# Optimization experiments

Measured on AMD Instinct MI355X. Metric: run time of the kernel, lower is better.

Reference implementation:

```python
import jax, jax.numpy as jnp
import numpy as np

B, T, H, IN, D = 256, 64, 256, 2, 8

def _gru_cell(x, h, Wih, Whh, bih, bhh):
    gi = x @ Wih.T + bih          # [B,3H]
    gh = h @ Whh.T + bhh
    ir, iz, inn = jnp.split(gi, 3, axis=-1)
    hr, hz, hn = jnp.split(gh, 3, axis=-1)
    r = jax.nn.sigmoid(ir + hr)
    z = jax.nn.sigmoid(iz + hz)
    n = jnp.tanh(inn + r * hn)
    return (1.0 - z) * n + z * h

def _gru2(x, h, p):
    # h: [2,B,H]; p: 8-tuple of layer-0 then layer-1 GRU params
    h0 = _gru_cell(x, h[0], p[0], p[1], p[2], p[3])
    h1 = _gru_cell(h0, h[1], p[4], p[5], p[6], p[7])
    return jnp.stack([h0, h1], axis=0)

def _attend(h_new, buf, i, attn_W, v_W, fc_W, fc_b):
    # h_new: [2,B,H] fresh RNN hidden; buf: [B,T,2,H] history of hiddens
    s = h_new.transpose(1, 0, 2)                            # [B,2,H]
    es = jnp.einsum('blh,gh->blg', s, attn_W[:, :H])        # s half of cat(s,hiddens)
    eh = jnp.einsum('bjlh,gh->bjlg', buf, attn_W[:, H:])    # hiddens half
    energy = jnp.tanh(es[:, None] + eh)                     # [B,T,2,H]
    logits = jnp.einsum('bjlg,og->bjlo', energy, v_W)       # [B,T,2,2]
    mask = (jnp.arange(buf.shape[1]) <= i)[None, :, None, None]
    logits = jnp.where(mask, logits, jnp.float32(-1e30))
    m = logits.max(axis=(1, 2), keepdims=True)              # softmax over all 2*(i+1) history slots
    e = jnp.exp(logits - m)
    a = e / e.sum(axis=(1, 2), keepdims=True)
    c = jnp.einsum('bjlo,bjlh->obh', a, buf)                # [2,B,H] == bmm(a,hiddens).transpose(0,1)
    h_cat = jnp.concatenate([c, h_new], axis=-1)            # [2,B,2H]
    return h_cat @ fc_W.T + fc_b                            # [2,B,H]

def setup_inputs():
    key = jax.random.key(0)
    ks = jax.random.split(key, 32)
    def u(k, shape, fan):
        b = 1.0 / np.sqrt(fan)
        return jax.random.uniform(k, shape, jnp.float32, -b, b)
    inp = {'received': jax.random.normal(ks[0], (B, T, IN), jnp.float32)}
    i = 1
    for g in ('g1', 'g2'):
        inp[g + '_Wih0'] = u(ks[i], (3 * H, IN), H); i += 1
        inp[g + '_Whh0'] = u(ks[i], (3 * H, H), H); i += 1
        inp[g + '_bih0'] = u(ks[i], (3 * H,), H); i += 1
        inp[g + '_bhh0'] = u(ks[i], (3 * H,), H); i += 1
        inp[g + '_Wih1'] = u(ks[i], (3 * H, H), H); i += 1
        inp[g + '_Whh1'] = u(ks[i], (3 * H, H), H); i += 1
        inp[g + '_bih1'] = u(ks[i], (3 * H,), H); i += 1
        inp[g + '_bhh1'] = u(ks[i], (3 * H,), H); i += 1
    inp['fc_W'] = u(ks[i], (H, 2 * H), 2 * H); i += 1
    inp['fc_b'] = u(ks[i], (H,), 2 * H); i += 1
    inp['attn_W'] = u(ks[i], (H, 2 * H), 2 * H); i += 1
    inp['v_W'] = u(ks[i], (2, H), H); i += 1
    inp['out_W'] = u(ks[i], (1, 2 * H), 2 * H); i += 1
    inp['out_b'] = u(ks[i], (1,), 2 * H); i += 1
    return inp

def reference(received, g1_Wih0, g1_Whh0, g1_bih0, g1_bhh0, g1_Wih1, g1_Whh1, g1_bih1, g1_bhh1,
              g2_Wih0, g2_Whh0, g2_bih0, g2_bhh0, g2_Wih1, g2_Whh1, g2_bih1, g2_bhh1,
              fc_W, fc_b, attn_W, v_W, out_W, out_b):
    p1 = (g1_Wih0, g1_Whh0, g1_bih0, g1_bhh0, g1_Wih1, g1_Whh1, g1_bih1, g1_bhh1)
    p2 = (g2_Wih0, g2_Whh0, g2_bih0, g2_bhh0, g2_Wih1, g2_Whh1, g2_bih1, g2_bhh1)
    b, t = received.shape[0], received.shape[1]
    h_init = jnp.zeros((2, b, H), received.dtype)
    buf_init = jnp.zeros((b, t, 2, H), received.dtype)

    def step(carry, inp):
        h1, h2, b1, b2 = carry
        x, i = inp
        h1n = _gru2(x, h1, p1)
        h2n = _gru2(x, h2, p2)
        b1 = b1.at[:, i].set(h1n.transpose(1, 0, 2))
        b2 = b2.at[:, i].set(h2n.transpose(1, 0, 2))
        h1a = _attend(h1n, b1, i, attn_W, v_W, fc_W, fc_b)
        h2a = _attend(h2n, b2, i, attn_W, v_W, fc_W, fc_b)
        return (h1a, h2a, b1, b2), (h1n[1], h2n[1])

    xs = (received.transpose(1, 0, 2), jnp.arange(t))
    _, (o1, o2) = jax.lax.scan(step, (h_init, h_init, buf_init, buf_init), xs)
    out1 = o1.transpose(1, 0, 2)   # [B,T,H] = concat of per-step top-layer GRU outputs
    out2 = o2.transpose(1, 0, 2)
    ar = jnp.arange(t)
    idx = jnp.where(ar >= t - D - 1, t - 1, ar + D)   # delayed stream-2 features
    rnn_out = jnp.concatenate([out1, out2[:, idx]], axis=-1)  # [B,T,2H]
    return jax.nn.sigmoid(rnn_out @ out_W.T + out_b)          # [B,T,1]
```

## Files before the change

### kernel.cpp

```cpp
#include <hip/hip_runtime.h>

#define BATCH 256
#define TT    64
#define HH    256
#define DD    8

#define BW    4
#define NTHR  1024
#define NBLK  (2 * (BATCH / BW))

#define CH48  24576
#define CH32  16384

typedef __attribute__((ext_vector_type(8))) short bfrag;
typedef __attribute__((ext_vector_type(4))) float f4;
typedef __attribute__((ext_vector_type(4))) unsigned int uv4;

#define SWZ(g) ((((g) & 31) << 3) | ((g) >> 5))

__device__ __forceinline__ float rcpf(float x) { return __builtin_amdgcn_rcpf(x); }
__device__ __forceinline__ float sigf(float x) { return rcpf(1.0f + __expf(-x)); }
__device__ __forceinline__ float tanh_fast(float x) {
  const float e = __expf(-2.0f * x);
  return __builtin_fmaf(2.0f, rcpf(1.0f + e), -1.0f);
}
__device__ __forceinline__ unsigned short f2bf(float f) {
  union { float f; unsigned int u; } v; v.f = f;
  return (unsigned short)((v.u + 0x7fffu + ((v.u >> 16) & 1u)) >> 16);
}
__device__ __forceinline__ float bf_lo(unsigned int u) {
  union { unsigned int u; float f; } v; v.u = u << 16; return v.f;
}
__device__ __forceinline__ float bf_hi(unsigned int u) {
  union { unsigned int u; float f; } v; v.u = u & 0xffff0000u; return v.f;
}
__device__ __forceinline__ bfrag zero_frag() {
  bfrag r;
#pragma unroll
  for (int x = 0; x < 8; x++) r[x] = 0;
  return r;
}
__device__ __forceinline__ f4 mfma16(bfrag a, bfrag b, f4 c) {
  return __builtin_amdgcn_mfma_f32_16x16x32_bf16(a, b, c, 0, 0, 0);
}

__device__ __forceinline__ void wait_vm(int n) {
  if (n == 0)      asm volatile("s_waitcnt vmcnt(0)" ::: "memory");
  else if (n == 2) asm volatile("s_waitcnt vmcnt(2)" ::: "memory");
  else if (n == 3) asm volatile("s_waitcnt vmcnt(3)" ::: "memory");
  else if (n == 6) asm volatile("s_waitcnt vmcnt(6)" ::: "memory");
  else             asm volatile("s_waitcnt vmcnt(7)" ::: "memory");
  __builtin_amdgcn_sched_barrier(0);
}
__device__ __forceinline__ void lds_release_bar() {
  asm volatile("s_waitcnt lgkmcnt(0)" ::: "memory");
  __builtin_amdgcn_sched_barrier(0);
  __builtin_amdgcn_s_barrier();
  __builtin_amdgcn_sched_barrier(0);
}

__device__ __forceinline__ void gl_lds16(const unsigned short* g, unsigned short* l) {
  __builtin_amdgcn_global_load_lds(
      (const __attribute__((address_space(1))) unsigned int*)g,
      (__attribute__((address_space(3))) unsigned int*)l, 16, 0, 0);
}
__device__ __forceinline__ void stage48(const unsigned short* g, unsigned short* l,
                                        int wave, int lane) {
#pragma unroll
  for (int r = 0; r < 3; ++r)
    gl_lds16(g + wave * 1536 + r * 512 + lane * 8, l + wave * 1536 + r * 512);
}
__device__ __forceinline__ void stage32(const unsigned short* g, unsigned short* l,
                                        int wave, int lane) {
#pragma unroll
  for (int r = 0; r < 2; ++r)
    gl_lds16(g + wave * 1024 + r * 512 + lane * 8, l + wave * 1024 + r * 512);
}

#define W1_ELEMS  196608
#define STACK_W   (3 * W1_ELEMS)
#define B3_OFF    (2 * STACK_W)
#define B4_OFF    (B3_OFF + 131072)
#define WF_TOTAL  (B4_OFF + 131072)

__global__ __launch_bounds__(256) void prep_weights(
    const float* __restrict__ g1_Whh0, const float* __restrict__ g1_Wih1, const float* __restrict__ g1_Whh1,
    const float* __restrict__ g2_Whh0, const float* __restrict__ g2_Wih1, const float* __restrict__ g2_Whh1,
    const float* __restrict__ attn_W, const float* __restrict__ fc_W,
    unsigned short* __restrict__ wf) {
  const int id = blockIdx.x * 256 + threadIdx.x;
  if (id >= WF_TOTAL) return;
  float src;
  if (id < 2 * STACK_W) {
    const int s = id / STACK_W, r = id % STACK_W;
    const int mm = r / W1_ELEMS, e = r % W1_ELEMS;
    const int c = e / CH48, e2 = e % CH48;
    const int wg = e2 >> 9, l8 = e2 & 511;
    const int w = wg / 3, g = wg % 3;
    const int lane = l8 >> 3, j = l8 & 7;
    const int n = w * 16 + (lane & 15);
    const int k = c * 32 + ((lane >> 4) << 3) + j;
    const float* W = (mm == 0) ? (s ? g2_Whh0 : g1_Whh0)
                   : (mm == 1) ? (s ? g2_Wih1 : g1_Wih1)
                               : (s ? g2_Whh1 : g1_Whh1);
    src = W[(g * 256 + n) * 256 + k];
  } else if (id < B4_OFF) {
    const int e = id - B3_OFF;
    const int c = e / CH32, e2 = e % CH32;
    const int t = e2 >> 9, l8 = e2 & 511;
    const int lane = l8 >> 3, j = l8 & 7;
    const int n = t * 16 + (lane & 15);
    const int k = c * 32 + ((lane >> 4) << 3) + j;
    src = (n < 256) ? attn_W[n * 512 + k] : attn_W[(n - 256) * 512 + 256 + k];
  } else {
    const int e = id - B4_OFF;
    const int cc = e / CH32, e2 = e % CH32;
    const int w = e2 >> 10, c2 = (e2 >> 9) & 1, l8 = e2 & 511;
    const int lane = l8 >> 3, j = l8 & 7;
    const int c = cc * 2 + c2;
    const int n = w * 16 + (lane & 15);
    const int k = c * 32 + ((lane >> 4) << 3) + j;
    src = fc_W[n * 512 + k];
  }
  wf[id] = f2bf(src);
}

__global__ __launch_bounds__(NTHR) void gru_attn(
    const float* __restrict__ received,
    const float* __restrict__ g1_Wih0, const float* __restrict__ g1_bih0, const float* __restrict__ g1_bhh0,
    const float* __restrict__ g1_bih1, const float* __restrict__ g1_bhh1,
    const float* __restrict__ g2_Wih0, const float* __restrict__ g2_bih0, const float* __restrict__ g2_bhh0,
    const float* __restrict__ g2_bih1, const float* __restrict__ g2_bhh1,
    const float* __restrict__ fc_b, const float* __restrict__ v_W, const float* __restrict__ out_W,
    const unsigned short* __restrict__ wf,
    unsigned short* __restrict__ buf_g, unsigned short* __restrict__ ehb_g,
    float* __restrict__ ws_p) {
  const int tid  = threadIdx.x;
  const int lane = tid & 63, wave = tid >> 6;
  const int col  = lane & 15, q = lane >> 4;
  const int s    = blockIdx.x & 1;
  const int b0   = (blockIdx.x >> 1) * BW;

  const float* Wih0 = s ? g2_Wih0 : g1_Wih0;
  const float* bih0 = s ? g2_bih0 : g1_bih0;
  const float* bhh0 = s ? g2_bhh0 : g1_bhh0;
  const float* bih1 = s ? g2_bih1 : g1_bih1;
  const float* bhh1 = s ? g2_bhh1 : g1_bhh1;

  const unsigned short* SR = wf + (size_t)s * STACK_W;
  const unsigned short* B3 = wf + B3_OFF;
  const unsigned short* B4 = wf + B4_OFF;

  unsigned short* buf = buf_g + (size_t)s * BATCH * TT * 2 * HH;
  unsigned short* ehb = ehb_g + (size_t)s * BATCH * TT * 2 * HH;
  float* pp = ws_p + (size_t)s * BATCH * TT;

  const int nm0 = wave * 16 + col;
  const float wxr0 = Wih0[nm0 * 2],         wxr1 = Wih0[nm0 * 2 + 1];
  const float wxz0 = Wih0[(256 + nm0) * 2], wxz1 = Wih0[(256 + nm0) * 2 + 1];
  const float wxn0 = Wih0[(512 + nm0) * 2], wxn1 = Wih0[(512 + nm0) * 2 + 1];
  const float br0  = bih0[nm0] + bhh0[nm0];
  const float bz0  = bih0[256 + nm0] + bhh0[256 + nm0];
  const float bni0 = bih0[512 + nm0], bnh0 = bhh0[512 + nm0];
  const float br1  = bih1[nm0] + bhh1[nm0];
  const float bz1  = bih1[256 + nm0] + bhh1[256 + nm0];
  const float bni1 = bih1[512 + nm0], bnh1 = bhh1[512 + nm0];
  const float fcb  = fc_b[nm0];
  const float owv  = out_W[s * HH + nm0];

  __shared__ float          hf[8 * 260] __attribute__((aligned(16)));
  __shared__ unsigned short hb[8 * 264] __attribute__((aligned(16)));
  __shared__ unsigned short hnb[8 * 264] __attribute__((aligned(16)));
  __shared__ float          es_s[8 * 264] __attribute__((aligned(16)));
  __shared__ unsigned short cacb[8 * 264] __attribute__((aligned(16)));
  __shared__ float          lp[TT * 4 * 2 * 2];
  __shared__ float          vw_s[512];
  __shared__ float          cpart[2 * 2 * 4 * 256] __attribute__((aligned(16)));
  __shared__ float          pw_s[64];
  __shared__ float          sinv_s[8];
  __shared__ float          xv_s[BW * TT * 2];
  __shared__ unsigned short wbuf[2][CH48] __attribute__((aligned(16)));

  for (int x = tid; x < 8 * 260; x += NTHR) hf[x] = 0.0f;
  for (int x = tid; x < 8 * 264; x += NTHR) hb[x] = 0;
  if (tid < 512) { const int o = tid >> 8, g = tid & 255; vw_s[o * 256 + SWZ(g)] = v_W[tid]; }
  if (tid < BW * TT * 2) {
    const int b = tid >> 7, r = tid & 127;
    xv_s[tid] = received[(size_t)(b0 + b) * TT * 2 + r];
  }
  __syncthreads();

  stage48(SR + 0 * CH48, wbuf[0], wave, lane);
  stage48(SR + 1 * CH48, wbuf[1], wave, lane);

#pragma unroll 1
  for (int i = 0; i < TT; ++i) {
    f4 aR = {0,0,0,0}, aZ = {0,0,0,0}, aN = {0,0,0,0};
#pragma unroll
    for (int c = 0; c < 8; ++c) {
      wait_vm(3);
      __builtin_amdgcn_s_barrier();
      __builtin_amdgcn_sched_barrier(0);
      const unsigned short* wb = wbuf[c & 1];
      const bfrag av = (col < BW) ? *(const bfrag*)&hb[col * 264 + c * 32 + q * 8] : zero_frag();
      const bfrag f0 = *(const bfrag*)&wb[(wave * 3 + 0) * 512 + lane * 8];
      const bfrag f1 = *(const bfrag*)&wb[(wave * 3 + 1) * 512 + lane * 8];
      const bfrag f2 = *(const bfrag*)&wb[(wave * 3 + 2) * 512 + lane * 8];
      aR = mfma16(av, f0, aR); aZ = mfma16(av, f1, aZ); aN = mfma16(av, f2, aN);
      lds_release_bar();
      stage48(SR + (c + 2) * CH48, wbuf[c & 1], wave, lane);
    }
    if (lane < 16) {
#pragma unroll
      for (int reg = 0; reg < 4; reg++) {
        const int b = reg;
        const float xr = xv_s[(b * TT + i) * 2 + 0];
        const float xi = xv_s[(b * TT + i) * 2 + 1];
        const float rr = sigf(xr * wxr0 + xi * wxr1 + br0 + aR[reg]);
        const float zz = sigf(xr * wxz0 + xi * wxz1 + bz0 + aZ[reg]);
        const float nn = tanh_fast(xr * wxn0 + xi * wxn1 + bni0 + rr * (aN[reg] + bnh0));
        const float hn0 = (1.0f - zz) * nn + zz * hf[b * 260 + nm0];
        const unsigned short hv = f2bf(hn0);
        hnb[b * 264 + nm0] = hv;
        buf[((size_t)(b0 + b) * (TT * 2) + i * 2 + 0) * HH + nm0] = hv;
      }
    }
    lds_release_bar();

    f4 iR = {0,0,0,0}, iZ = {0,0,0,0}, iN = {0,0,0,0};
#pragma unroll
    for (int c = 8; c < 16; ++c) {
      wait_vm(c < 10 ? 7 : 3);
      __builtin_amdgcn_s_barrier();
      __builtin_amdgcn_sched_barrier(0);
      const unsigned short* wb = wbuf[c & 1];
      const bfrag av = (col < BW) ? *(const bfrag*)&hnb[col * 264 + (c - 8) * 32 + q * 8] : zero_frag();
      const bfrag f0 = *(const bfrag*)&wb[(wave * 3 + 0) * 512 + lane * 8];
      const bfrag f1 = *(const bfrag*)&wb[(wave * 3 + 1) * 512 + lane * 8];
      const bfrag f2 = *(const bfrag*)&wb[(wave * 3 + 2) * 512 + lane * 8];
      iR = mfma16(av, f0, iR); iZ = mfma16(av, f1, iZ); iN = mfma16(av, f2, iN);
      lds_release_bar();
      stage48(SR + (c + 2) * CH48, wbuf[c & 1], wave, lane);
    }

    f4 hR = {0,0,0,0}, hZ = {0,0,0,0}, hN = {0,0,0,0};
#pragma unroll
    for (int c = 16; c < 24; ++c) {
      wait_vm(c < 23 ? 3 : 0);
      __builtin_amdgcn_s_barrier();
      __builtin_amdgcn_sched_barrier(0);
      const unsigned short* wb = wbuf[c & 1];
      const bfrag av = (col < BW) ? *(const bfrag*)&hb[(4 + col) * 264 + (c - 16) * 32 + q * 8] : zero_frag();
      const bfrag f0 = *(const bfrag*)&wb[(wave * 3 + 0) * 512 + lane * 8];
      const bfrag f1 = *(const bfrag*)&wb[(wave * 3 + 1) * 512 + lane * 8];
      const bfrag f2 = *(const bfrag*)&wb[(wave * 3 + 2) * 512 + lane * 8];
      hR = mfma16(av, f0, hR); hZ = mfma16(av, f1, hZ); hN = mfma16(av, f2, hN);
      lds_release_bar();
      if (c + 2 < 24) stage48(SR + (c + 2) * CH48, wbuf[c & 1], wave, lane);
    }
    stage32(B3 + 0 * CH32, wbuf[0], wave, lane);
    stage32(B3 + 1 * CH32, wbuf[1], wave, lane);
    {
      float pv[4] = {0.f, 0.f, 0.f, 0.f};
      if (lane < 16) {
#pragma unroll
        for (int reg = 0; reg < 4; reg++) {
          const int b = reg;
          const float rr = sigf(iR[reg] + hR[reg] + br1);
          const float zz = sigf(iZ[reg] + hZ[reg] + bz1);
          const float nn = tanh_fast(iN[reg] + bni1 + rr * (hN[reg] + bnh1));
          const float hn1 = (1.0f - zz) * nn + zz * hf[(4 + b) * 260 + nm0];
          const unsigned short hv = f2bf(hn1);
          hnb[(4 + b) * 264 + nm0] = hv;
          buf[((size_t)(b0 + b) * (TT * 2) + i * 2 + 1) * HH + nm0] = hv;
          pv[reg] += hn1 * owv;
        }
      }
#pragma unroll
      for (int reg = 0; reg < 4; reg++) {
#pragma unroll
        for (int d = 1; d < 16; d <<= 1) pv[reg] += __shfl_xor(pv[reg], d, 64);
      }
      if (lane == 0) {
#pragma unroll
        for (int reg = 0; reg < 4; reg++) pw_s[wave * 4 + reg] = pv[reg];
      }
    }
    lds_release_bar();

    {
      f4 ac0 = {0,0,0,0}, ac1 = {0,0,0,0};
#pragma unroll
      for (int c = 0; c < 8; ++c) {
        wait_vm(c < 2 ? 6 : (c < 7 ? 2 : 0));
        __builtin_amdgcn_s_barrier();
        __builtin_amdgcn_sched_barrier(0);
        const unsigned short* wb = wbuf[c & 1];
        const bfrag av = (col < 8) ? *(const bfrag*)&hnb[col * 264 + c * 32 + q * 8] : zero_frag();
        const bfrag f0 = *(const bfrag*)&wb[(2 * wave + 0) * 512 + lane * 8];
        const bfrag f1 = *(const bfrag*)&wb[(2 * wave + 1) * 512 + lane * 8];
        ac0 = mfma16(av, f0, ac0);
        ac1 = mfma16(av, f1, ac1);
        lds_release_bar();
        if (c + 2 < 8) stage32(B3 + (c + 2) * CH32, wbuf[c & 1], wave, lane);
      }
#pragma unroll
      for (int tt = 0; tt < 2; tt++) {
        const f4 acc = tt ? ac1 : ac0;
        const int t = wave * 2 + tt;
        if (lane < 32) {
          const int n = t * 16 + col;
#pragma unroll
          for (int reg = 0; reg < 4; reg++) {
            const int m = q * 4 + reg;
            const int l = m >> 2, b = m & 3;
            if (t < 16) es_s[(b * 2 + l) * 264 + SWZ(n)] = acc[reg];
            else ehb[((size_t)(b0 + b) * (TT * 2) + i * 2 + l) * HH + (n - 256)] = f2bf(acc[reg]);
          }
        }
      }
      if (tid < 4) {
        float ss = 0.0f;
#pragma unroll
        for (int w = 0; w < 16; w++) ss += pw_s[w * 4 + tid];
        pp[(size_t)(b0 + tid) * TT + i] = ss;
      }
    }
    __syncthreads();

    {
      const int nslot = 64 * (i + 1);
      int slot = tid;
      uv4 cur[4];
      if (slot < nslot) {
        const uv4* ep = (const uv4*)(ehb + ((size_t)(b0 + ((slot >> 3) & 3)) * (TT * 2) +
                                            (slot >> 6) * 2 + ((slot >> 5) & 1)) * HH + (slot & 7) * 32);
#pragma unroll
        for (int u = 0; u < 4; u++) cur[u] = __builtin_nontemporal_load(ep + u);
      }
      for (; slot < nslot; slot += NTHR) {
        const int snext = slot + NTHR;
        uv4 nxt[4];
        if (snext < nslot) {
          const uv4* ep2 = (const uv4*)(ehb + ((size_t)(b0 + ((snext >> 3) & 3)) * (TT * 2) +
                                               (snext >> 6) * 2 + ((snext >> 5) & 1)) * HH + (snext & 7) * 32);
#pragma unroll
          for (int u = 0; u < 4; u++) nxt[u] = __builtin_nontemporal_load(ep2 + u);
        } else {
#pragma unroll
          for (int u = 0; u < 4; u++) nxt[u] = cur[u];
        }
        const int g8 = slot & 7;
        const int b  = (slot >> 3) & 3;
        const int l  = (slot >> 5) & 1;
        const int j  = slot >> 6;
        const int eb = (b * 2 + l) * 264;
        float l0 = 0.0f, l1 = 0.0f;
#pragma unroll
        for (int u = 0; u < 4; u++) {
#pragma unroll
          for (int k = 0; k < 4; k++) {
            const int m = u * 8 + k * 2;
            const float e0 = tanh_fast(es_s[eb + (m * 8 + g8)] + bf_lo(cur[u][k]));
            const float e1 = tanh_fast(es_s[eb + ((m + 1) * 8 + g8)] + bf_hi(cur[u][k]));
            l0 = fmaf(e0, vw_s[m * 8 + g8], fmaf(e1, vw_s[(m + 1) * 8 + g8], l0));
            l1 = fmaf(e0, vw_s[256 + m * 8 + g8], fmaf(e1, vw_s[256 + (m + 1) * 8 + g8], l1));
          }
        }
#pragma unroll
        for (int d = 1; d < 8; d <<= 1) { l0 += __shfl_xor(l0, d, 64); l1 += __shfl_xor(l1, d, 64); }
        if (g8 == 0) {
          lp[((j * 4 + b) * 2 + l) * 2 + 0] = __expf(l0);
          lp[((j * 4 + b) * 2 + l) * 2 + 1] = __expf(l1);
        }
#pragma unroll
        for (int u = 0; u < 4; u++) cur[u] = nxt[u];
      }
    }
    __syncthreads();

    {
      if (wave < 8) {
        const int b = wave >> 1, o = wave & 1;
        const int jl2 = 2 * (i + 1);
        const int jl0 = lane, jl1 = lane + 64;
        float sa = 0.0f;
        if (jl0 < jl2) sa += lp[((jl0 >> 1) * 4 + b) * 4 + (jl0 & 1) * 2 + o];
        if (jl1 < jl2) sa += lp[((jl1 >> 1) * 4 + b) * 4 + (jl1 & 1) * 2 + o];
#pragma unroll
        for (int d = 1; d < 64; d <<= 1) sa += __shfl_xor(sa, d, 64);
        if (lane == 0) sinv_s[b * 2 + o] = rcpf(sa);
      }
      const int h2   = tid & 127;
      const int jpar = (tid >> 7) & 1;
      const int cb   = tid >> 8;
      const unsigned int* bp = (const unsigned int*)(buf + ((size_t)(b0 + cb) * (TT * 2)) * HH);
      float c00 = 0.f, c01 = 0.f, c10 = 0.f, c11 = 0.f;
      unsigned int aj0 = 0, aj1 = 0, bj0 = 0, bj1 = 0;
      int j = jpar;
      if (j <= i) {
        aj0 = __builtin_nontemporal_load(bp + (j * 2 + 0) * 128 + h2);
        aj1 = __builtin_nontemporal_load(bp + (j * 2 + 1) * 128 + h2);
        bj0 = __builtin_nontemporal_load(bp + ((j + 2) * 2 + 0) * 128 + h2);
        bj1 = __builtin_nontemporal_load(bp + ((j + 2) * 2 + 1) * 128 + h2);
      }
      for (; j <= i; j += 2) {
        unsigned int cj0 = 0, cj1 = 0;
        if (j + 4 <= i) {
          cj0 = __builtin_nontemporal_load(bp + ((j + 4) * 2 + 0) * 128 + h2);
          cj1 = __builtin_nontemporal_load(bp + ((j + 4) * 2 + 1) * 128 + h2);
        }
#pragma unroll
        for (int l = 0; l < 2; l++) {
          const unsigned int u = l ? aj1 : aj0;
          const float e0 = lp[((j * 4 + cb) * 2 + l) * 2 + 0];
          const float e1 = lp[((j * 4 + cb) * 2 + l) * 2 + 1];
          const float v0 = bf_lo(u), v1 = bf_hi(u);
          c00 = fmaf(e0, v0, c00); c01 = fmaf(e0, v1, c01);
          c10 = fmaf(e1, v0, c10); c11 = fmaf(e1, v1, c11);
        }
        aj0 = bj0; aj1 = bj1; bj0 = cj0; bj1 = cj1;
      }
      ((float2*)&cpart[((jpar * 2 + 0) * 4 + cb) * 256])[h2] = make_float2(c00, c01);
      ((float2*)&cpart[((jpar * 2 + 1) * 4 + cb) * 256])[h2] = make_float2(c10, c11);
    }
    __syncthreads();

    stage32(B4 + 0 * CH32, wbuf[0], wave, lane);
    stage32(B4 + 1 * CH32, wbuf[1], wave, lane);
    for (int x = tid; x < 2 * BW * HH; x += NTHR) {
      const int g = x & 255, b = (x >> 8) & 3, o = x >> 10;
      const float v = (cpart[((0 * 2 + o) * 4 + b) * 256 + g] +
                       cpart[((1 * 2 + o) * 4 + b) * 256 + g]) *
                      sinv_s[b * 2 + o];
      cacb[(o * 4 + b) * 264 + g] = f2bf(v);
    }
    __syncthreads();

    {
      f4 acc = {0, 0, 0, 0};
#pragma unroll
      for (int cc = 0; cc < 8; ++cc) {
        wait_vm(cc < 7 ? 2 : 0);
        __builtin_amdgcn_s_barrier();
        __builtin_amdgcn_sched_barrier(0);
        const unsigned short* wb = wbuf[cc & 1];
        bfrag a0v, a1v;
        if (col < 8) {
          a0v = (cc < 4) ? *(const bfrag*)&cacb[col * 264 + cc * 64 + q * 8]
                         : *(const bfrag*)&hnb[col * 264 + (cc - 4) * 64 + q * 8];
          a1v = (cc < 4) ? *(const bfrag*)&cacb[col * 264 + cc * 64 + 32 + q * 8]
                         : *(const bfrag*)&hnb[col * 264 + (cc - 4) * 64 + 32 + q * 8];
        } else { a0v = zero_frag(); a1v = zero_frag(); }
        const bfrag g0 = *(const bfrag*)&wb[(wave * 2 + 0) * 512 + lane * 8];
        const bfrag g1 = *(const bfrag*)&wb[(wave * 2 + 1) * 512 + lane * 8];
        acc = mfma16(a0v, g0, acc);
        acc = mfma16(a1v, g1, acc);
        lds_release_bar();
        if (cc + 2 < 8) stage32(B4 + (cc + 2) * CH32, wbuf[cc & 1], wave, lane);
      }
      if (i + 1 < TT) {
        stage48(SR + 0 * CH48, wbuf[0], wave, lane);
        stage48(SR + 1 * CH48, wbuf[1], wave, lane);
      }
      if (lane < 32) {
#pragma unroll
        for (int reg = 0; reg < 4; reg++) {
          const int m = q * 4 + reg;
          const float v = acc[reg] + fcb;
          hf[m * 260 + nm0] = v;
          hb[m * 264 + nm0] = f2bf(v);
        }
      }
    }
    lds_release_bar();
  }
}

__global__ __launch_bounds__(256) void final_combine(const float* __restrict__ ws_p,
                                                     const float* __restrict__ out_b,
                                                     float* __restrict__ out) {
  const int gidx = blockIdx.x * blockDim.x + threadIdx.x;
  if (gidx >= BATCH * TT) return;
  const int b = gidx >> 6;
  const int t = gidx & 63;
  const int idx = (t >= TT - DD - 1) ? (TT - 1) : (t + DD);
  const float* p1 = ws_p;
  const float* p2 = ws_p + (size_t)BATCH * TT;
  const float v = p1[(size_t)b * TT + t] + p2[(size_t)b * TT + idx] + out_b[0];
  out[gidx] = 1.0f / (1.0f + __expf(-v));
}

extern "C" void kernel_launch(void* const* d_in, const int* in_sizes, int n_in,
                              void* d_out, int out_size, void* d_ws, size_t ws_size,
                              hipStream_t stream) {
  const float* received = (const float*)d_in[0];
  const float* g1_Wih0 = (const float*)d_in[1];
  const float* g1_Whh0 = (const float*)d_in[2];
  const float* g1_bih0 = (const float*)d_in[3];
  const float* g1_bhh0 = (const float*)d_in[4];
  const float* g1_Wih1 = (const float*)d_in[5];
  const float* g1_Whh1 = (const float*)d_in[6];
  const float* g1_bih1 = (const float*)d_in[7];
  const float* g1_bhh1 = (const float*)d_in[8];
  const float* g2_Wih0 = (const float*)d_in[9];
  const float* g2_Whh0 = (const float*)d_in[10];
  const float* g2_bih0 = (const float*)d_in[11];
  const float* g2_bhh0 = (const float*)d_in[12];
  const float* g2_Wih1 = (const float*)d_in[13];
  const float* g2_Whh1 = (const float*)d_in[14];
  const float* g2_bih1 = (const float*)d_in[15];
  const float* g2_bhh1 = (const float*)d_in[16];
  const float* fc_W   = (const float*)d_in[17];
  const float* fc_b   = (const float*)d_in[18];
  const float* attn_W = (const float*)d_in[19];
  const float* v_W    = (const float*)d_in[20];
  const float* out_W  = (const float*)d_in[21];
  const float* out_b  = (const float*)d_in[22];

  float* ws_p = (float*)d_ws;
  unsigned short* buf = (unsigned short*)(ws_p + 2 * BATCH * TT);
  unsigned short* ehb = buf + (size_t)2 * BATCH * TT * 2 * HH;
  unsigned short* wf  = ehb + (size_t)2 * BATCH * TT * 2 * HH;

  hipLaunchKernelGGL(prep_weights, dim3((WF_TOTAL + 255) / 256), dim3(256), 0, stream,
                     g1_Whh0, g1_Wih1, g1_Whh1, g2_Whh0, g2_Wih1, g2_Whh1,
                     attn_W, fc_W, wf);

  hipLaunchKernelGGL(gru_attn, dim3(NBLK), dim3(NTHR), 0, stream,
                     received,
                     g1_Wih0, g1_bih0, g1_bhh0, g1_bih1, g1_bhh1,
                     g2_Wih0, g2_bih0, g2_bhh0, g2_bih1, g2_bhh1,
                     fc_b, v_W, out_W, wf, buf, ehb, ws_p);

  hipLaunchKernelGGL(final_combine, dim3((BATCH * TT + 255) / 256), dim3(256), 0, stream,
                     ws_p, out_b, (float*)d_out);
}
```

Baseline: 6.193 ms.

## Drop per-chunk workgroup barriers in weight streaming and deepen history prefetch

Removes the s_barrier and LDS-release barrier around every weight chunk in the GRU and FC MFMA loops. This relies on each wave staging and consuming only its own slice of the double-buffered LDS weights, so only per-wave vmcnt waits remain. The next-stage weight prefetches now start after the block-wide barriers instead of before them, which keeps them from overwriting buffers other waves may still be reading. Separately, the attention-context loop now keeps four history rows of nontemporal loads in flight instead of two, and several __syncthreads become lighter LDS release barriers. The risk is a cross-wave race if any wave reads LDS data that another wave staged.

```diff
diff --git a/kernel.cpp b/kernel.cpp
--- a/kernel.cpp
+++ b/kernel.cpp
@@ -48,7 +48,6 @@
   if (n == 0)      asm volatile("s_waitcnt vmcnt(0)" ::: "memory");
   else if (n == 2) asm volatile("s_waitcnt vmcnt(2)" ::: "memory");
   else if (n == 3) asm volatile("s_waitcnt vmcnt(3)" ::: "memory");
-  else if (n == 6) asm volatile("s_waitcnt vmcnt(6)" ::: "memory");
   else             asm volatile("s_waitcnt vmcnt(7)" ::: "memory");
   __builtin_amdgcn_sched_barrier(0);
 }
@@ -199,15 +198,13 @@
 #pragma unroll
     for (int c = 0; c < 8; ++c) {
       wait_vm(3);
-      __builtin_amdgcn_s_barrier();
-      __builtin_amdgcn_sched_barrier(0);
       const unsigned short* wb = wbuf[c & 1];
       const bfrag av = (col < BW) ? *(const bfrag*)&hb[col * 264 + c * 32 + q * 8] : zero_frag();
       const bfrag f0 = *(const bfrag*)&wb[(wave * 3 + 0) * 512 + lane * 8];
       const bfrag f1 = *(const bfrag*)&wb[(wave * 3 + 1) * 512 + lane * 8];
       const bfrag f2 = *(const bfrag*)&wb[(wave * 3 + 2) * 512 + lane * 8];
       aR = mfma16(av, f0, aR); aZ = mfma16(av, f1, aZ); aN = mfma16(av, f2, aN);
-      lds_release_bar();
+      __builtin_amdgcn_sched_barrier(0);
       stage48(SR + (c + 2) * CH48, wbuf[c & 1], wave, lane);
     }
     if (lane < 16) {
@@ -231,15 +228,13 @@
 #pragma unroll
     for (int c = 8; c < 16; ++c) {
       wait_vm(c < 10 ? 7 : 3);
-      __builtin_amdgcn_s_barrier();
-      __builtin_amdgcn_sched_barrier(0);
       const unsigned short* wb = wbuf[c & 1];
       const bfrag av = (col < BW) ? *(const bfrag*)&hnb[col * 264 + (c - 8) * 32 + q * 8] : zero_frag();
       const bfrag f0 = *(const bfrag*)&wb[(wave * 3 + 0) * 512 + lane * 8];
       const bfrag f1 = *(const bfrag*)&wb[(wave * 3 + 1) * 512 + lane * 8];
       const bfrag f2 = *(const bfrag*)&wb[(wave * 3 + 2) * 512 + lane * 8];
       iR = mfma16(av, f0, iR); iZ = mfma16(av, f1, iZ); iN = mfma16(av, f2, iN);
-      lds_release_bar();
+      __builtin_amdgcn_sched_barrier(0);
       stage48(SR + (c + 2) * CH48, wbuf[c & 1], wave, lane);
     }
 
@@ -247,19 +242,15 @@
 #pragma unroll
     for (int c = 16; c < 24; ++c) {
       wait_vm(c < 23 ? 3 : 0);
-      __builtin_amdgcn_s_barrier();
-      __builtin_amdgcn_sched_barrier(0);
       const unsigned short* wb = wbuf[c & 1];
       const bfrag av = (col < BW) ? *(const bfrag*)&hb[(4 + col) * 264 + (c - 16) * 32 + q * 8] : zero_frag();
       const bfrag f0 = *(const bfrag*)&wb[(wave * 3 + 0) * 512 + lane * 8];
       const bfrag f1 = *(const bfrag*)&wb[(wave * 3 + 1) * 512 + lane * 8];
       const bfrag f2 = *(const bfrag*)&wb[(wave * 3 + 2) * 512 + lane * 8];
       hR = mfma16(av, f0, hR); hZ = mfma16(av, f1, hZ); hN = mfma16(av, f2, hN);
-      lds_release_bar();
+      __builtin_amdgcn_sched_barrier(0);
       if (c + 2 < 24) stage48(SR + (c + 2) * CH48, wbuf[c & 1], wave, lane);
     }
-    stage32(B3 + 0 * CH32, wbuf[0], wave, lane);
-    stage32(B3 + 1 * CH32, wbuf[1], wave, lane);
     {
       float pv[4] = {0.f, 0.f, 0.f, 0.f};
       if (lane < 16) {
@@ -287,21 +278,21 @@
       }
     }
     lds_release_bar();
+    stage32(B3 + 0 * CH32, wbuf[0], wave, lane);
+    stage32(B3 + 1 * CH32, wbuf[1], wave, lane);
 
     {
       f4 ac0 = {0,0,0,0}, ac1 = {0,0,0,0};
 #pragma unroll
       for (int c = 0; c < 8; ++c) {
-        wait_vm(c < 2 ? 6 : (c < 7 ? 2 : 0));
-        __builtin_amdgcn_s_barrier();
-        __builtin_amdgcn_sched_barrier(0);
+        wait_vm(c < 7 ? 2 : 0);
         const unsigned short* wb = wbuf[c & 1];
         const bfrag av = (col < 8) ? *(const bfrag*)&hnb[col * 264 + c * 32 + q * 8] : zero_frag();
         const bfrag f0 = *(const bfrag*)&wb[(2 * wave + 0) * 512 + lane * 8];
         const bfrag f1 = *(const bfrag*)&wb[(2 * wave + 1) * 512 + lane * 8];
         ac0 = mfma16(av, f0, ac0);
         ac1 = mfma16(av, f1, ac1);
-        lds_release_bar();
+        __builtin_amdgcn_sched_barrier(0);
         if (c + 2 < 8) stage32(B3 + (c + 2) * CH32, wbuf[c & 1], wave, lane);
       }
 #pragma unroll
@@ -377,7 +368,7 @@
         for (int u = 0; u < 4; u++) cur[u] = nxt[u];
       }
     }
-    __syncthreads();
+    lds_release_bar();
 
     {
       if (wave < 8) {
@@ -396,35 +387,41 @@
       const int cb   = tid >> 8;
       const unsigned int* bp = (const unsigned int*)(buf + ((size_t)(b0 + cb) * (TT * 2)) * HH);
       float c00 = 0.f, c01 = 0.f, c10 = 0.f, c11 = 0.f;
-      unsigned int aj0 = 0, aj1 = 0, bj0 = 0, bj1 = 0;
+      unsigned int a0v = 0, a1v = 0, b0v = 0, b1v = 0;
+      unsigned int c0v = 0, c1v = 0, d0v = 0, d1v = 0;
       int j = jpar;
       if (j <= i) {
-        aj0 = __builtin_nontemporal_load(bp + (j * 2 + 0) * 128 + h2);
-        aj1 = __builtin_nontemporal_load(bp + (j * 2 + 1) * 128 + h2);
-        bj0 = __builtin_nontemporal_load(bp + ((j + 2) * 2 + 0) * 128 + h2);
-        bj1 = __builtin_nontemporal_load(bp + ((j + 2) * 2 + 1) * 128 + h2);
+        a0v = __builtin_nontemporal_load(bp + (j * 2 + 0) * 128 + h2);
+        a1v = __builtin_nontemporal_load(bp + (j * 2 + 1) * 128 + h2);
+        b0v = __builtin_nontemporal_load(bp + ((j + 2) * 2 + 0) * 128 + h2);
+        b1v = __builtin_nontemporal_load(bp + ((j + 2) * 2 + 1) * 128 + h2);
+        c0v = __builtin_nontemporal_load(bp + ((j + 4) * 2 + 0) * 128 + h2);
+        c1v = __builtin_nontemporal_load(bp + ((j + 4) * 2 + 1) * 128 + h2);
+        d0v = __builtin_nontemporal_load(bp + ((j + 6) * 2 + 0) * 128 + h2);
+        d1v = __builtin_nontemporal_load(bp + ((j + 6) * 2 + 1) * 128 + h2);
       }
       for (; j <= i; j += 2) {
-        unsigned int cj0 = 0, cj1 = 0;
-        if (j + 4 <= i) {
-          cj0 = __builtin_nontemporal_load(bp + ((j + 4) * 2 + 0) * 128 + h2);
-          cj1 = __builtin_nontemporal_load(bp + ((j + 4) * 2 + 1) * 128 + h2);
+        unsigned int e0v = 0, e1v = 0;
+        if (j + 8 <= i) {
+          e0v = __builtin_nontemporal_load(bp + ((j + 8) * 2 + 0) * 128 + h2);
+          e1v = __builtin_nontemporal_load(bp + ((j + 8) * 2 + 1) * 128 + h2);
         }
 #pragma unroll
         for (int l = 0; l < 2; l++) {
-          const unsigned int u = l ? aj1 : aj0;
+          const unsigned int u = l ? a1v : a0v;
           const float e0 = lp[((j * 4 + cb) * 2 + l) * 2 + 0];
           const float e1 = lp[((j * 4 + cb) * 2 + l) * 2 + 1];
           const float v0 = bf_lo(u), v1 = bf_hi(u);
           c00 = fmaf(e0, v0, c00); c01 = fmaf(e0, v1, c01);
           c10 = fmaf(e1, v0, c10); c11 = fmaf(e1, v1, c11);
         }
-        aj0 = bj0; aj1 = bj1; bj0 = cj0; bj1 = cj1;
+        a0v = b0v; a1v = b1v; b0v = c0v; b1v = c1v;
+        c0v = d0v; c1v = d1v; d0v = e0v; d1v = e1v;
       }
       ((float2*)&cpart[((jpar * 2 + 0) * 4 + cb) * 256])[h2] = make_float2(c00, c01);
       ((float2*)&cpart[((jpar * 2 + 1) * 4 + cb) * 256])[h2] = make_float2(c10, c11);
     }
-    __syncthreads();
+    lds_release_bar();
 
     stage32(B4 + 0 * CH32, wbuf[0], wave, lane);
     stage32(B4 + 1 * CH32, wbuf[1], wave, lane);
@@ -435,33 +432,27 @@
                       sinv_s[b * 2 + o];
       cacb[(o * 4 + b) * 264 + g] = f2bf(v);
     }
-    __syncthreads();
+    lds_release_bar();
 
     {
       f4 acc = {0, 0, 0, 0};
 #pragma unroll
       for (int cc = 0; cc < 8; ++cc) {
         wait_vm(cc < 7 ? 2 : 0);
-        __builtin_amdgcn_s_barrier();
-        __builtin_amdgcn_sched_barrier(0);
         const unsigned short* wb = wbuf[cc & 1];
-        bfrag a0v, a1v;
+        bfrag a0f, a1f;
         if (col < 8) {
-          a0v = (cc < 4) ? *(const bfrag*)&cacb[col * 264 + cc * 64 + q * 8]
+          a0f = (cc < 4) ? *(const bfrag*)&cacb[col * 264 + cc * 64 + q * 8]
                          : *(const bfrag*)&hnb[col * 264 + (cc - 4) * 64 + q * 8];
-          a1v = (cc < 4) ? *(const bfrag*)&cacb[col * 264 + cc * 64 + 32 + q * 8]
+          a1f = (cc < 4) ? *(const bfrag*)&cacb[col * 264 + cc * 64 + 32 + q * 8]
                          : *(const bfrag*)&hnb[col * 264 + (cc - 4) * 64 + 32 + q * 8];
-        } else { a0v = zero_frag(); a1v = zero_frag(); }
+        } else { a0f = zero_frag(); a1f = zero_frag(); }
         const bfrag g0 = *(const bfrag*)&wb[(wave * 2 + 0) * 512 + lane * 8];
         const bfrag g1 = *(const bfrag*)&wb[(wave * 2 + 1) * 512 + lane * 8];
-        acc = mfma16(a0v, g0, acc);
-        acc = mfma16(a1v, g1, acc);
-        lds_release_bar();
+        acc = mfma16(a0f, g0, acc);
+        acc = mfma16(a1f, g1, acc);
+        __builtin_amdgcn_sched_barrier(0);
         if (cc + 2 < 8) stage32(B4 + (cc + 2) * CH32, wbuf[cc & 1], wave, lane);
-      }
-      if (i + 1 < TT) {
-        stage48(SR + 0 * CH48, wbuf[0], wave, lane);
-        stage48(SR + 1 * CH48, wbuf[1], wave, lane);
       }
       if (lane < 32) {
 #pragma unroll
@@ -474,6 +465,10 @@
       }
     }
     lds_release_bar();
+    if (i + 1 < TT) {
+      stage48(SR + 0 * CH48, wbuf[0], wave, lane);
+      stage48(SR + 1 * CH48, wbuf[1], wave, lane);
+    }
   }
 }
 
```

Result: faster. 5.713 ms (-7.7%).
